# Kernel tuning notes

Hardware: AMD Instinct MI355X
Metric: run time of the kernel (lower is better)

Reference implementation:

```python
import jax, jax.numpy as jnp
import numpy as np


def setup_inputs() -> dict:
    key = jax.random.key(0)
    k1, k2 = jax.random.split(key)
    B, Lq, Lk, D = 4, 4096, 4096, 512
    query = jax.random.normal(k1, (B, Lq, D), dtype=jnp.float32)
    value = jax.random.normal(k2, (B, Lk, D), dtype=jnp.float32)
    return {"query": query, "value": value}


def reference(query, value):
    # score: [B, Lq, Lk] = query @ value^T (unscaled, unmasked)
    score = jnp.einsum('bqd,bkd->bqk', query, value)
    attn = jax.nn.softmax(score, axis=-1)
    # context: [B, Lq, D]
    context = jnp.einsum('bqk,bkd->bqd', attn, value)
    return (context, attn)
```

## Files before the change

### kernel.cpp

```cpp
#include <hip/hip_runtime.h>
#include <cstddef>
#include <cstdint>

typedef unsigned short u16;

constexpr int BATCH = 4;
constexpr int Lq = 4096;
constexpr int Lk = 4096;
constexpr int D  = 512;

constexpr int BM = 128, BN = 128, BK = 32;
constexpr int LDA = 40;

using bf16x8 = __attribute__((ext_vector_type(8))) short;
using f32x4  = __attribute__((ext_vector_type(4))) float;

__device__ inline u16 f32_to_bf16_rne(float x) {
    uint32_t u = __builtin_bit_cast(uint32_t, x);
    u += 0x7fff + ((u >> 16) & 1);
    return (u16)(u >> 16);
}
__device__ inline float bf16_bits_to_f32(u16 h) {
    uint32_t u = ((uint32_t)h) << 16;
    return __builtin_bit_cast(float, u);
}
__device__ inline void split2(float x, float y, uint32_t& hi, uint32_t& lo) {
    u16 hx = f32_to_bf16_rne(x);
    u16 hy = f32_to_bf16_rne(y);
    u16 lx = f32_to_bf16_rne(x - bf16_bits_to_f32(hx));
    u16 ly = f32_to_bf16_rne(y - bf16_bits_to_f32(hy));
    hi = (uint32_t)hx | ((uint32_t)hy << 16);
    lo = (uint32_t)lx | ((uint32_t)ly << 16);
}
__device__ inline uint32_t pack2_bf16(float x, float y) {
    return (uint32_t)f32_to_bf16_rne(x) | ((uint32_t)f32_to_bf16_rne(y) << 16);
}
__device__ inline void gld16(const u16* g, u16* l) {
    __builtin_amdgcn_global_load_lds(
        (const __attribute__((address_space(1))) void*)g,
        (__attribute__((address_space(3))) void*)l, 16, 0, 0);
}
__device__ inline f32x4 mfma16(bf16x8 a, bf16x8 b, f32x4 c) {
    return __builtin_amdgcn_mfma_f32_16x16x32_bf16(a, b, c, 0, 0, 0);
}

__global__ __launch_bounds__(256)
void split_qv_bf16(const float* __restrict__ Q, const float* __restrict__ V,
                   u16* __restrict__ Qhi, u16* __restrict__ Qlo,
                   u16* __restrict__ Vhi, u16* __restrict__ Vlo, int n4)
{
    int i = blockIdx.x * 256 + threadIdx.x;
    const float* src;
    u16 *hi, *lo;
    if (i < n4) { src = Q; hi = Qhi; lo = Qlo; }
    else        { src = V; hi = Vhi; lo = Vlo; i -= n4; }
    const float4 v = ((const float4*)src)[i];
    uint2 h, l;
    split2(v.x, v.y, h.x, l.x);
    split2(v.z, v.w, h.y, l.y);
    ((uint2*)hi)[i] = h;
    ((uint2*)lo)[i] = l;
}

__global__ __launch_bounds__(256)
void transpose_v_bf16(const float* __restrict__ V, u16* __restrict__ VT)
{
    __shared__ float tile[32][33];
    const int b = blockIdx.z;
    const float* in = V + (size_t)b * Lk * D;
    u16* out = VT + (size_t)b * D * Lk;
    const int lk0 = blockIdx.x * 32;
    const int d0  = blockIdx.y * 32;
    const int c  = threadIdx.x & 31;
    const int r0 = threadIdx.x >> 5;
    #pragma unroll
    for (int i = 0; i < 4; ++i) {
        const int r = r0 + 8 * i;
        tile[r][c] = in[(size_t)(lk0 + r) * D + d0 + c];
    }
    __syncthreads();
    #pragma unroll
    for (int i = 0; i < 4; ++i) {
        const int r = r0 + 8 * i;
        out[(size_t)(d0 + r) * Lk + lk0 + c] = f32_to_bf16_rne(tile[c][r]);
    }
}

__global__ __launch_bounds__(512, 2)
void gemm1_8p(const u16* __restrict__ Qhi, const u16* __restrict__ Qlo,
              const u16* __restrict__ Vhi, const u16* __restrict__ Vlo,
              float* __restrict__ Sg)
{
    constexpr int K  = D;
    constexpr int NT = K / 32;
    __shared__ u16 lds[2 * 4 * 8192];

    const int b = blockIdx.z;
    const u16* Ah = Qhi + (size_t)b * Lq * K;
    const u16* Al = Qlo + (size_t)b * Lq * K;
    const u16* Bh = Vhi + (size_t)b * Lk * K;
    const u16* Bl = Vlo + (size_t)b * Lk * K;
    float* C = Sg + (size_t)b * Lq * Lk;

    const int m0 = blockIdx.y * 256;
    const int n0 = blockIdx.x * 256;
    const int t = threadIdx.x, lane = t & 63, w = t >> 6;
    const int wm = (w >> 2) * 128, wn = (w & 3) * 64;
    const int fr = lane & 15, fq = lane >> 4;

    const int cg   = (lane & 3) ^ ((lane >> 3) & 3);
    const int rsub = lane >> 2;
    const int offA0 = (m0 + w * 32 + rsub) * K + cg * 8;
    const int offA1 = offA0 + 16 * K;
    const int offB0 = (n0 + w * 32 + rsub) * K + cg * 8;
    const int offB1 = offB0 + 16 * K;
    const int ch = w * 1024;

    const int swzc = fq ^ ((fr >> 1) & 3);
    const int aRd = (wm + fr) * 64 + swzc * 16;
    const int bRd = (wn + fr) * 64 + swzc * 16;

    f32x4 acc[8][4] = {};
    bf16x8 aH[4], aL[4], bH[4], bL[4];

    {
        u16* a = &lds[ch];
        gld16(Ah + offA0, a);
        gld16(Ah + offA1, a + 512);
        gld16(Al + offA0, a + 8192);
        gld16(Al + offA1, a + 8192 + 512);
        u16* v = &lds[16384 + ch];
        gld16(Bh + offB0, v);
        gld16(Bh + offB1, v + 512);
        gld16(Bl + offB0, v + 8192);
        gld16(Bl + offB1, v + 8192 + 512);
    }
    asm volatile("s_waitcnt vmcnt(0)" ::: "memory");
    __builtin_amdgcn_s_barrier();
    __builtin_amdgcn_sched_barrier(0);

    for (int kt = 0; kt < NT; ++kt) {
        const int cur = kt & 1;
        const char* ls = (const char*)lds + cur * 65536;
        const int kn = (kt + 1) * 32;
        const int nb = (cur ^ 1) * 32768;

        #pragma unroll
        for (int m = 0; m < 4; ++m) {
            aH[m] = *(const bf16x8*)(ls + aRd + m * 1024);
            aL[m] = *(const bf16x8*)(ls + 16384 + aRd + m * 1024);
        }
        #pragma unroll
        for (int n = 0; n < 2; ++n) {
            bH[n] = *(const bf16x8*)(ls + 32768 + bRd + n * 1024);
            bL[n] = *(const bf16x8*)(ls + 49152 + bRd + n * 1024);
        }
        if (kt < NT - 1) {
            u16* a = &lds[nb + ch];
            gld16(Ah + offA0 + kn, a);
            gld16(Ah + offA1 + kn, a + 512);
            gld16(Al + offA0 + kn, a + 8192);
            gld16(Al + offA1 + kn, a + 8192 + 512);
        }
        __builtin_amdgcn_s_barrier();
        asm volatile("s_waitcnt lgkmcnt(0)" ::: "memory");
        __builtin_amdgcn_sched_barrier(0);
        __builtin_amdgcn_s_setprio(1);
        #pragma unroll
        for (int m = 0; m < 4; ++m)
            #pragma unroll
            for (int n = 0; n < 2; ++n) {
                acc[m][n] = mfma16(aH[m], bH[n], acc[m][n]);
                acc[m][n] = mfma16(aH[m], bL[n], acc[m][n]);
                acc[m][n] = mfma16(aL[m], bH[n], acc[m][n]);
            }
        __builtin_amdgcn_s_setprio(0);
        __builtin_amdgcn_s_barrier();
        __builtin_amdgcn_sched_barrier(0);

        #pragma unroll
        for (int n = 2; n < 4; ++n) {
            bH[n] = *(const bf16x8*)(ls + 32768 + bRd + n * 1024);
            bL[n] = *(const bf16x8*)(ls + 49152 + bRd + n * 1024);
        }
        if (kt < NT - 1) {
            u16* v = &lds[nb + 16384 + ch];
            gld16(Bh + offB0 + kn, v);
            gld16(Bh + offB1 + kn, v + 512);
            gld16(Bl + offB0 + kn, v + 8192);
            gld16(Bl + offB1 + kn, v + 8192 + 512);
        }
        __builtin_amdgcn_s_barrier();
        asm volatile("s_waitcnt lgkmcnt(0)" ::: "memory");
        __builtin_amdgcn_sched_barrier(0);
        __builtin_amdgcn_s_setprio(1);
        #pragma unroll
        for (int m = 0; m < 4; ++m)
            #pragma unroll
            for (int n = 2; n < 4; ++n) {
                acc[m][n] = mfma16(aH[m], bH[n], acc[m][n]);
                acc[m][n] = mfma16(aH[m], bL[n], acc[m][n]);
                acc[m][n] = mfma16(aL[m], bH[n], acc[m][n]);
            }
        __builtin_amdgcn_s_setprio(0);
        __builtin_amdgcn_s_barrier();
        __builtin_amdgcn_sched_barrier(0);

        #pragma unroll
        for (int m = 0; m < 4; ++m) {
            aH[m] = *(const bf16x8*)(ls + 4096 + aRd + m * 1024);
            aL[m] = *(const bf16x8*)(ls + 16384 + 4096 + aRd + m * 1024);
        }
        __builtin_amdgcn_s_barrier();
        asm volatile("s_waitcnt lgkmcnt(0)" ::: "memory");
        __builtin_amdgcn_sched_barrier(0);
        __builtin_amdgcn_s_setprio(1);
        #pragma unroll
        for (int m = 0; m < 4; ++m)
            #pragma unroll
            for (int n = 0; n < 2; ++n) {
                acc[4 + m][n] = mfma16(aH[m], bH[n], acc[4 + m][n]);
                acc[4 + m][n] = mfma16(aH[m], bL[n], acc[4 + m][n]);
                acc[4 + m][n] = mfma16(aL[m], bH[n], acc[4 + m][n]);
            }
        __builtin_amdgcn_s_setprio(0);
        __builtin_amdgcn_s_barrier();
        __builtin_amdgcn_sched_barrier(0);

        __builtin_amdgcn_s_setprio(1);
        #pragma unroll
        for (int m = 0; m < 4; ++m)
            #pragma unroll
            for (int n = 2; n < 4; ++n) {
                acc[4 + m][n] = mfma16(aH[m], bH[n], acc[4 + m][n]);
                acc[4 + m][n] = mfma16(aH[m], bL[n], acc[4 + m][n]);
                acc[4 + m][n] = mfma16(aL[m], bH[n], acc[4 + m][n]);
            }
        __builtin_amdgcn_s_setprio(0);
        asm volatile("s_waitcnt vmcnt(0)" ::: "memory");
        __builtin_amdgcn_s_barrier();
        __builtin_amdgcn_sched_barrier(0);
    }

    const int rowb = m0 + wm + fq * 4;
    const int colb = n0 + wn + fr;
    #pragma unroll
    for (int mi = 0; mi < 8; ++mi)
        #pragma unroll
        for (int ni = 0; ni < 4; ++ni)
            #pragma unroll
            for (int r = 0; r < 4; ++r)
                C[(size_t)(rowb + mi * 16 + r) * Lk + colb + ni * 16] = acc[mi][ni][r];
}

__global__ __launch_bounds__(256)
void softmax_wave(float* __restrict__ S, u16* __restrict__ Pb)
{
    const size_t row = (size_t)blockIdx.x * 4 + (threadIdx.x >> 6);
    const int l = threadIdx.x & 63;
    float* p = S + row * (size_t)Lk;

    float4 v[16];
    #pragma unroll
    for (int j = 0; j < 16; ++j) v[j] = ((const float4*)p)[l + j * 64];

    float m = -3.0e38f;
    #pragma unroll
    for (int j = 0; j < 16; ++j)
        m = fmaxf(m, fmaxf(fmaxf(v[j].x, v[j].y), fmaxf(v[j].z, v[j].w)));
    #pragma unroll
    for (int off = 32; off > 0; off >>= 1) m = fmaxf(m, __shfl_xor(m, off));

    float s = 0.f;
    #pragma unroll
    for (int j = 0; j < 16; ++j) {
        v[j].x = __expf(v[j].x - m); s += v[j].x;
        v[j].y = __expf(v[j].y - m); s += v[j].y;
        v[j].z = __expf(v[j].z - m); s += v[j].z;
        v[j].w = __expf(v[j].w - m); s += v[j].w;
    }
    #pragma unroll
    for (int off = 32; off > 0; off >>= 1) s += __shfl_xor(s, off);

    const float inv = 1.0f / s;
    u16* prow = Pb ? Pb + row * (size_t)Lk : nullptr;
    #pragma unroll
    for (int j = 0; j < 16; ++j) {
        v[j].x *= inv; v[j].y *= inv; v[j].z *= inv; v[j].w *= inv;
        ((float4*)p)[l + j * 64] = v[j];
        if (prow) {
            ushort4 h = make_ushort4(f32_to_bf16_rne(v[j].x), f32_to_bf16_rne(v[j].y),
                                     f32_to_bf16_rne(v[j].z), f32_to_bf16_rne(v[j].w));
            ((ushort4*)prow)[l + j * 64] = h;
        }
    }
}

__global__ __launch_bounds__(256, 3)
void gemm2_mfma(const u16* __restrict__ Pg, const u16* __restrict__ VTg,
                float* __restrict__ Cg)
{
    constexpr int K = Lk;
    constexpr int N = D;
    __shared__ u16 sA[BM * 64];
    __shared__ u16 sB[BN * 64];

    const int b = blockIdx.z;
    const u16* A  = Pg  + (size_t)b * Lq * Lk;
    const u16* Bp = VTg + (size_t)b * (size_t)D * Lk;
    float* C = Cg + (size_t)b * Lq * D;

    const int m0 = blockIdx.y * BM;
    const int n0 = blockIdx.x * BN;
    const int t = threadIdx.x, lane = t & 63, wave = t >> 6;
    const int wm = (wave >> 1) * 64, wn = (wave & 1) * 64;
    const int fr = lane & 15, fq = lane >> 4;

    const int lr  = lane >> 3;
    const int gck = (lane & 7) ^ lr;
    const int gA  = (m0 + wave * 32 + lr) * K + gck * 8;
    const int gB  = (n0 + wave * 32 + lr) * K + gck * 8;

    f32x4 acc[4][4] = {};

    for (int k0 = 0; k0 < K; k0 += 64) {
        if (k0) __syncthreads();
        #pragma unroll
        for (int j = 0; j < 4; ++j) {
            gld16(A  + gA + j * 8 * K + k0, &sA[(wave * 4 + j) * 512]);
            gld16(Bp + gB + j * 8 * K + k0, &sB[(wave * 4 + j) * 512]);
        }
        __syncthreads();

        #pragma unroll
        for (int ks = 0; ks < 2; ++ks) {
            bf16x8 af[4], bf[4];
            #pragma unroll
            for (int x = 0; x < 4; ++x) {
                const int ra = wm + x * 16 + fr;
                const int rb = wn + x * 16 + fr;
                af[x] = *(const bf16x8*)&sA[ra * 64 + ((ks * 4 + fq) ^ (ra & 7)) * 8];
                bf[x] = *(const bf16x8*)&sB[rb * 64 + ((ks * 4 + fq) ^ (rb & 7)) * 8];
            }
            #pragma unroll
            for (int mi = 0; mi < 4; ++mi)
                #pragma unroll
                for (int ni = 0; ni < 4; ++ni)
                    acc[mi][ni] = mfma16(af[mi], bf[ni], acc[mi][ni]);
        }
    }

    #pragma unroll
    for (int mi = 0; mi < 4; ++mi)
        #pragma unroll
        for (int ni = 0; ni < 4; ++ni)
            #pragma unroll
            for (int r = 0; r < 4; ++r) {
                const int row = m0 + wm + mi * 16 + fq * 4 + r;
                const int col = n0 + wn + ni * 16 + fr;
                C[(size_t)row * N + col] = acc[mi][ni][r];
            }
}

__global__ __launch_bounds__(256, 2)
void gemm1_r2(const float* __restrict__ Qg, const float* __restrict__ Vg,
              float* __restrict__ Sg)
{
    constexpr int K = D;
    __shared__ alignas(16) u16 sAhi[BM * LDA];
    __shared__ alignas(16) u16 sAlo[BM * LDA];
    __shared__ alignas(16) u16 sBhi[BN * LDA];
    __shared__ alignas(16) u16 sBlo[BN * LDA];

    const int b = blockIdx.z;
    const float* A  = Qg + (size_t)b * Lq * D;
    const float* Bp = Vg + (size_t)b * Lk * D;
    float* C = Sg + (size_t)b * Lq * Lk;

    const int m0 = blockIdx.y * BM;
    const int n0 = blockIdx.x * BN;
    const int t = threadIdx.x, lane = t & 63, wave = t >> 6;
    const int wm = (wave >> 1) * 64, wn = (wave & 1) * 64;
    const int fr = lane & 15, fq = lane >> 4;
    const int sm = t >> 3, sc = t & 7;

    f32x4 acc[4][4] = {};

    for (int k0 = 0; k0 < K; k0 += BK) {
        if (k0) __syncthreads();
        #pragma unroll
        for (int i = 0; i < 4; ++i) {
            const int m = sm + 32 * i;
            const float4 va = *(const float4*)(A  + (size_t)(m0 + m) * K + k0 + sc * 4);
            const float4 vb = *(const float4*)(Bp + (size_t)(n0 + m) * K + k0 + sc * 4);
            uint2 h, l;
            split2(va.x, va.y, h.x, l.x);
            split2(va.z, va.w, h.y, l.y);
            *(uint2*)&sAhi[m * LDA + sc * 4] = h;
            *(uint2*)&sAlo[m * LDA + sc * 4] = l;
            split2(vb.x, vb.y, h.x, l.x);
            split2(vb.z, vb.w, h.y, l.y);
            *(uint2*)&sBhi[m * LDA + sc * 4] = h;
            *(uint2*)&sBlo[m * LDA + sc * 4] = l;
        }
        __syncthreads();

        bf16x8 ah[4], al[4], bh[4], bl[4];
        #pragma unroll
        for (int x = 0; x < 4; ++x) {
            ah[x] = *(const bf16x8*)&sAhi[(wm + x * 16 + fr) * LDA + fq * 8];
            al[x] = *(const bf16x8*)&sAlo[(wm + x * 16 + fr) * LDA + fq * 8];
            bh[x] = *(const bf16x8*)&sBhi[(wn + x * 16 + fr) * LDA + fq * 8];
            bl[x] = *(const bf16x8*)&sBlo[(wn + x * 16 + fr) * LDA + fq * 8];
        }
        #pragma unroll
        for (int mi = 0; mi < 4; ++mi)
            #pragma unroll
            for (int ni = 0; ni < 4; ++ni) {
                acc[mi][ni] = __builtin_amdgcn_mfma_f32_16x16x32_bf16(ah[mi], bh[ni], acc[mi][ni], 0, 0, 0);
                acc[mi][ni] = __builtin_amdgcn_mfma_f32_16x16x32_bf16(ah[mi], bl[ni], acc[mi][ni], 0, 0, 0);
                acc[mi][ni] = __builtin_amdgcn_mfma_f32_16x16x32_bf16(al[mi], bh[ni], acc[mi][ni], 0, 0, 0);
            }
    }

    #pragma unroll
    for (int mi = 0; mi < 4; ++mi)
        #pragma unroll
        for (int ni = 0; ni < 4; ++ni)
            #pragma unroll
            for (int r = 0; r < 4; ++r) {
                const int row = m0 + wm + mi * 16 + fq * 4 + r;
                const int col = n0 + wn + ni * 16 + fr;
                C[(size_t)row * Lk + col] = acc[mi][ni][r];
            }
}

__global__ __launch_bounds__(256, 2)
void gemm2_r2(const float* __restrict__ Pg, const u16* __restrict__ VTg,
              float* __restrict__ Cg)
{
    constexpr int K = Lk;
    constexpr int N = D;
    __shared__ alignas(16) u16 sA[BM * LDA];
    __shared__ alignas(16) u16 sB[BN * LDA];

    const int b = blockIdx.z;
    const float* A  = Pg  + (size_t)b * Lq * Lk;
    const u16*   Bp = VTg + (size_t)b * (size_t)D * Lk;
    float* C = Cg + (size_t)b * Lq * D;

    const int m0 = blockIdx.y * BM;
    const int n0 = blockIdx.x * BN;
    const int t = threadIdx.x, lane = t & 63, wave = t >> 6;
    const int wm = (wave >> 1) * 64, wn = (wave & 1) * 64;
    const int fr = lane & 15, fq = lane >> 4;
    const int sm = t >> 3, sc = t & 7;
    const int bn = t >> 2, bc = t & 3;

    f32x4 acc[4][4] = {};

    for (int k0 = 0; k0 < K; k0 += BK) {
        if (k0) __syncthreads();
        #pragma unroll
        for (int i = 0; i < 4; ++i) {
            const int m = sm + 32 * i;
            const float4 va = *(const float4*)(A + (size_t)(m0 + m) * K + k0 + sc * 4);
            uint2 h;
            h.x = pack2_bf16(va.x, va.y);
            h.y = pack2_bf16(va.z, va.w);
            *(uint2*)&sA[m * LDA + sc * 4] = h;
        }
        #pragma unroll
        for (int i = 0; i < 2; ++i) {
            const int n = bn + 64 * i;
            const bf16x8 vb = *(const bf16x8*)(Bp + (size_t)(n0 + n) * K + k0 + bc * 8);
            *(bf16x8*)&sB[n * LDA + bc * 8] = vb;
        }
        __syncthreads();

        bf16x8 af[4], bf[4];
        #pragma unroll
        for (int x = 0; x < 4; ++x) {
            af[x] = *(const bf16x8*)&sA[(wm + x * 16 + fr) * LDA + fq * 8];
            bf[x] = *(const bf16x8*)&sB[(wn + x * 16 + fr) * LDA + fq * 8];
        }
        #pragma unroll
        for (int mi = 0; mi < 4; ++mi)
            #pragma unroll
            for (int ni = 0; ni < 4; ++ni)
                acc[mi][ni] = __builtin_amdgcn_mfma_f32_16x16x32_bf16(af[mi], bf[ni], acc[mi][ni], 0, 0, 0);
    }

    #pragma unroll
    for (int mi = 0; mi < 4; ++mi)
        #pragma unroll
        for (int ni = 0; ni < 4; ++ni)
            #pragma unroll
            for (int r = 0; r < 4; ++r) {
                const int row = m0 + wm + mi * 16 + fq * 4 + r;
                const int col = n0 + wn + ni * 16 + fr;
                C[(size_t)row * N + col] = acc[mi][ni][r];
            }
}

extern "C" void kernel_launch(void* const* d_in, const int* in_sizes, int n_in,
                              void* d_out, int out_size, void* d_ws, size_t ws_size,
                              hipStream_t stream)
{
    const float* Q = (const float*)d_in[0];
    const float* V = (const float*)d_in[1];
    float* ctx  = (float*)d_out;
    float* attn = (float*)d_out + (size_t)BATCH * Lq * D;

    constexpr size_t NQ = (size_t)BATCH * Lq * D;
    constexpr size_t NP = (size_t)BATCH * Lq * Lk;
    const size_t need = (5 * NQ + NP) * sizeof(u16);

    if (ws_size >= need) {
        u16* Qhi = (u16*)d_ws;
        u16* Qlo = Qhi + NQ;
        u16* Vhi = Qlo + NQ;
        u16* Vlo = Vhi + NQ;
        u16* VT  = Vlo + NQ;
        u16* Pb  = VT  + NQ;

        const int n4 = (int)(NQ / 4);
        split_qv_bf16<<<dim3(2 * n4 / 256), 256, 0, stream>>>(Q, V, Qhi, Qlo, Vhi, Vlo, n4);
        transpose_v_bf16<<<dim3(Lk / 32, D / 32, BATCH), 256, 0, stream>>>(V, VT);
        gemm1_8p<<<dim3(Lk / 256, Lq / 256, BATCH), 512, 0, stream>>>(Qhi, Qlo, Vhi, Vlo, attn);
        softmax_wave<<<dim3(BATCH * Lq / 4), 256, 0, stream>>>(attn, Pb);
        gemm2_mfma<<<dim3(D / BN, Lq / BM, BATCH), 256, 0, stream>>>(Pb, VT, ctx);
    } else {
        u16* VT = (u16*)d_ws;
        transpose_v_bf16<<<dim3(Lk / 32, D / 32, BATCH), 256, 0, stream>>>(V, VT);
        gemm1_r2<<<dim3(Lk / BN, Lq / BM, BATCH), 256, 0, stream>>>(Q, V, attn);
        softmax_wave<<<dim3(BATCH * Lq / 4), 256, 0, stream>>>(attn, nullptr);
        gemm2_r2<<<dim3(D / BN, Lq / BM, BATCH), 256, 0, stream>>>(attn, VT, ctx);
    }
}
```

Before: 727.0 us.

## Fuse softmax normalization into PV GEMM using precomputed row statistics

Splits softmax into a stats-only pass that writes per-row max and reciprocal sum. A new fused kernel recomputes exp, writes the normalized attn back to global memory, converts it to bf16 in LDS and runs the PV MFMA over a full 512-wide D tile per 32-row block. This removes the bf16 P write/read round trip and the separate softmax write pass. In exchange the scores are read twice, occupancy is limited by the large LDS footprint (64KB for V^T), and V^T is re-streamed for every 32-row tile with no multi-buffering.

```diff
diff --git a/kernel.cpp b/kernel.cpp
--- a/kernel.cpp
+++ b/kernel.cpp
@@ -254,6 +254,125 @@
 }
 
 __global__ __launch_bounds__(256)
+void row_stats(const float* __restrict__ S, float* __restrict__ rowM,
+               float* __restrict__ rowI)
+{
+    const size_t row = (size_t)blockIdx.x * 4 + (threadIdx.x >> 6);
+    const int l = threadIdx.x & 63;
+    const float* p = S + row * (size_t)Lk;
+
+    float4 v[16];
+    #pragma unroll
+    for (int j = 0; j < 16; ++j) v[j] = ((const float4*)p)[l + j * 64];
+
+    float m = -3.0e38f;
+    #pragma unroll
+    for (int j = 0; j < 16; ++j)
+        m = fmaxf(m, fmaxf(fmaxf(v[j].x, v[j].y), fmaxf(v[j].z, v[j].w)));
+    #pragma unroll
+    for (int off = 32; off > 0; off >>= 1) m = fmaxf(m, __shfl_xor(m, off));
+
+    float s = 0.f;
+    #pragma unroll
+    for (int j = 0; j < 16; ++j) {
+        s += __expf(v[j].x - m);
+        s += __expf(v[j].y - m);
+        s += __expf(v[j].z - m);
+        s += __expf(v[j].w - m);
+    }
+    #pragma unroll
+    for (int off = 32; off > 0; off >>= 1) s += __shfl_xor(s, off);
+
+    if (l == 0) {
+        rowM[row] = m;
+        rowI[row] = 1.0f / s;
+    }
+}
+
+__global__ __launch_bounds__(512, 4)
+void fused_pv(float* __restrict__ S, const u16* __restrict__ VTg,
+              float* __restrict__ ctx, const float* __restrict__ rowM,
+              const float* __restrict__ rowI)
+{
+    constexpr int NT = Lk / 64;
+    __shared__ u16 sB[512 * 64];
+    __shared__ u16 sA[32 * 64];
+
+    const int i = blockIdx.x;
+    const int b = (i >> 1) & 3;
+    const int rt = ((i >> 3) << 1) | (i & 1);
+    const int m0 = rt * 32;
+
+    float* Srow = S + ((size_t)b * Lq + m0) * Lk;
+    const u16* VT = VTg + (size_t)b * (size_t)D * Lk;
+    float* C = ctx + ((size_t)b * Lq + m0) * D;
+
+    const int t = threadIdx.x, lane = t & 63, w = t >> 6;
+    const int fr = lane & 15, fq = lane >> 4;
+
+    const int srow = t >> 4;
+    const int sk = (t & 15) * 4;
+    const float mrow = rowM[(size_t)b * Lq + m0 + srow];
+    const float inv  = rowI[(size_t)b * Lq + m0 + srow];
+    const int aw = srow * 64 + (((sk >> 3) ^ (srow & 7)) * 8) + (sk & 4);
+
+    const int vrow = w * 8 + (lane >> 3);
+    const int vck = (lane & 7) ^ (lane >> 3);
+    const int swc = fr & 7;
+
+    f32x4 acc[2][4] = {};
+
+    for (int kt = 0; kt < NT; ++kt) {
+        const int k0 = kt * 64;
+        if (kt) __syncthreads();
+
+        #pragma unroll
+        for (int j = 0; j < 8; ++j)
+            gld16(VT + (size_t)(j * 64 + vrow) * Lk + k0 + vck * 8,
+                  &sB[(j * 512 + w * 64) * 8]);
+
+        float4 v = *(const float4*)(Srow + (size_t)srow * Lk + k0 + sk);
+        v.x = __expf(v.x - mrow) * inv;
+        v.y = __expf(v.y - mrow) * inv;
+        v.z = __expf(v.z - mrow) * inv;
+        v.w = __expf(v.w - mrow) * inv;
+        *(float4*)(Srow + (size_t)srow * Lk + k0 + sk) = v;
+        uint2 h;
+        h.x = pack2_bf16(v.x, v.y);
+        h.y = pack2_bf16(v.z, v.w);
+        *(uint2*)&sA[aw] = h;
+
+        __syncthreads();
+
+        #pragma unroll
+        for (int ks = 0; ks < 2; ++ks) {
+            const int pc = (ks * 4 + fq) ^ swc;
+            bf16x8 af[2], bf[4];
+            #pragma unroll
+            for (int x = 0; x < 2; ++x)
+                af[x] = *(const bf16x8*)&sA[(x * 16 + fr) * 64 + pc * 8];
+            #pragma unroll
+            for (int x = 0; x < 4; ++x)
+                bf[x] = *(const bf16x8*)&sB[(w * 64 + x * 16 + fr) * 64 + pc * 8];
+            #pragma unroll
+            for (int mi = 0; mi < 2; ++mi)
+                #pragma unroll
+                for (int ni = 0; ni < 4; ++ni)
+                    acc[mi][ni] = mfma16(af[mi], bf[ni], acc[mi][ni]);
+        }
+    }
+
+    #pragma unroll
+    for (int mi = 0; mi < 2; ++mi)
+        #pragma unroll
+        for (int ni = 0; ni < 4; ++ni)
+            #pragma unroll
+            for (int r = 0; r < 4; ++r)
+                C[(size_t)(mi * 16 + fq * 4 + r) * D + w * 64 + ni * 16 + fr] =
+                    acc[mi][ni][r];
+}
+
+__global__ __launch_bounds__(256)
 void softmax_wave(float* __restrict__ S, u16* __restrict__ Pb)
 {
     const size_t row = (size_t)blockIdx.x * 4 + (threadIdx.x >> 6);
@@ -294,72 +413,6 @@
             ((ushort4*)prow)[l + j * 64] = h;
         }
     }
-}
-
-__global__ __launch_bounds__(256, 3)
-void gemm2_mfma(const u16* __restrict__ Pg, const u16* __restrict__ VTg,
-                float* __restrict__ Cg)
-{
-    constexpr int K = Lk;
-    constexpr int N = D;
-    __shared__ u16 sA[BM * 64];
-    __shared__ u16 sB[BN * 64];
-
-    const int b = blockIdx.z;
-    const u16* A  = Pg  + (size_t)b * Lq * Lk;
-    const u16* Bp = VTg + (size_t)b * (size_t)D * Lk;
-    float* C = Cg + (size_t)b * Lq * D;
-
-    const int m0 = blockIdx.y * BM;
-    const int n0 = blockIdx.x * BN;
-    const int t = threadIdx.x, lane = t & 63, wave = t >> 6;
-    const int wm = (wave >> 1) * 64, wn = (wave & 1) * 64;
-    const int fr = lane & 15, fq = lane >> 4;
-
-    const int lr  = lane >> 3;
-    const int gck = (lane & 7) ^ lr;
-    const int gA  = (m0 + wave * 32 + lr) * K + gck * 8;
-    const int gB  = (n0 + wave * 32 + lr) * K + gck * 8;
-
-    f32x4 acc[4][4] = {};
-
-    for (int k0 = 0; k0 < K; k0 += 64) {
-        if (k0) __syncthreads();
-        #pragma unroll
-        for (int j = 0; j < 4; ++j) {
-            gld16(A  + gA + j * 8 * K + k0, &sA[(wave * 4 + j) * 512]);
-            gld16(Bp + gB + j * 8 * K + k0, &sB[(wave * 4 + j) * 512]);
-        }
-        __syncthreads();
-
-        #pragma unroll
-        for (int ks = 0; ks < 2; ++ks) {
-            bf16x8 af[4], bf[4];
-            #pragma unroll
-            for (int x = 0; x < 4; ++x) {
-                const int ra = wm + x * 16 + fr;
-                const int rb = wn + x * 16 + fr;
-                af[x] = *(const bf16x8*)&sA[ra * 64 + ((ks * 4 + fq) ^ (ra & 7)) * 8];
-                bf[x] = *(const bf16x8*)&sB[rb * 64 + ((ks * 4 + fq) ^ (rb & 7)) * 8];
-            }
-            #pragma unroll
-            for (int mi = 0; mi < 4; ++mi)
-                #pragma unroll
-                for (int ni = 0; ni < 4; ++ni)
-                    acc[mi][ni] = mfma16(af[mi], bf[ni], acc[mi][ni]);
-        }
-    }
-
-    #pragma unroll
-    for (int mi = 0; mi < 4; ++mi)
-        #pragma unroll
-        for (int ni = 0; ni < 4; ++ni)
-            #pragma unroll
-            for (int r = 0; r < 4; ++r) {
-                const int row = m0 + wm + mi * 16 + fq * 4 + r;
-                const int col = n0 + wn + ni * 16 + fr;
-                C[(size_t)row * N + col] = acc[mi][ni][r];
-            }
 }
 
 __global__ __launch_bounds__(256, 2)
@@ -524,12 +577,15 @@
         u16* VT  = Vlo + NQ;
         u16* Pb  = VT  + NQ;
 
+        float* rowM = (float*)Pb;
+        float* rowI = rowM + (size_t)BATCH * Lq;
+
         const int n4 = (int)(NQ / 4);
         split_qv_bf16<<<dim3(2 * n4 / 256), 256, 0, stream>>>(Q, V, Qhi, Qlo, Vhi, Vlo, n4);
         transpose_v_bf16<<<dim3(Lk / 32, D / 32, BATCH), 256, 0, stream>>>(V, VT);
         gemm1_8p<<<dim3(Lk / 256, Lq / 256, BATCH), 512, 0, stream>>>(Qhi, Qlo, Vhi, Vlo, attn);
-        softmax_wave<<<dim3(BATCH * Lq / 4), 256, 0, stream>>>(attn, Pb);
-        gemm2_mfma<<<dim3(D / BN, Lq / BM, BATCH), 256, 0, stream>>>(Pb, VT, ctx);
+        row_stats<<<dim3(BATCH * Lq / 4), 256, 0, stream>>>(attn, rowM, rowI);
+        fused_pv<<<dim3(512), 512, 0, stream>>>(attn, VT, ctx, rowM, rowI);
     } else {
         u16* VT = (u16*)d_ws;
         transpose_v_bf16<<<dim3(Lk / 32, D / 32, BATCH), 256, 0, stream>>>(V, VT);
```

Result: slower. 770.1 us (+5.9%).
